# Kernel tuning notes

Measured on AMD Instinct MI355X. Metric: run time of the kernel, lower is better.

## Reference

```python
import jax, jax.numpy as jnp
import numpy as np
from jax import lax

NUM_CLASSES = 2
TOP_K = 200
CONF_THRESH = 0.01
NMS_THRESH = 0.45
VAR0, VAR1 = 0.1, 0.2  # SSD cfg['variance']
BATCH, NUM_PRIORS = 8, 4096


def setup_inputs() -> dict:
    key = jax.random.key(0)
    k1, k2, k3, k4 = jax.random.split(key, 4)
    loc_data = jax.random.normal(k1, (BATCH, NUM_PRIORS, 4), dtype=jnp.float32)
    conf_data = jax.random.normal(k2, (BATCH * NUM_PRIORS, NUM_CLASSES), dtype=jnp.float32)
    # priors: (cx, cy, w, h), centers in [0,1], sizes in [0.02, 0.3]
    centers = jax.random.uniform(k3, (NUM_PRIORS, 2), dtype=jnp.float32)
    sizes = jax.random.uniform(k4, (NUM_PRIORS, 2), dtype=jnp.float32, minval=0.02, maxval=0.3)
    prior_data = jnp.concatenate([centers, sizes], axis=1)
    return {"loc_data": loc_data, "conf_data": conf_data, "prior_data": prior_data}


def _pairwise_iou(boxes):
    # boxes: [N, 4] in (x1, y1, x2, y2)
    x1, y1, x2, y2 = boxes[:, 0], boxes[:, 1], boxes[:, 2], boxes[:, 3]
    area = (x2 - x1) * (y2 - y1)
    iw = jnp.maximum(jnp.minimum(x2[:, None], x2[None, :]) - jnp.maximum(x1[:, None], x1[None, :]), 0.0)
    ih = jnp.maximum(jnp.minimum(y2[:, None], y2[None, :]) - jnp.maximum(y1[:, None], y1[None, :]), 0.0)
    inter = iw * ih
    return inter / (area[:, None] + area[None, :] - inter)


def _nms_image(boxes, scores):
    # boxes [N,4], scores [N] -> [TOP_K, 5] rows of (score, x1, y1, x2, y2)
    N = scores.shape[0]
    order = jnp.argsort(-scores)
    b = boxes[order]
    s = scores[order]
    valid = s > CONF_THRESH  # conf threshold (c_mask in torch code)
    iou = _pairwise_iou(b)  # [N, N]

    def step(suppressed, xs):
        i, row, v = xs
        kept_i = v & jnp.logical_not(suppressed[i])
        suppressed = suppressed | (kept_i & (row > NMS_THRESH))
        return suppressed, kept_i

    _, kept = lax.scan(step, jnp.zeros((N,), bool), (jnp.arange(N), iou, valid))
    # scatter kept rows (in descending-score order) into the first <=TOP_K slots
    pos = jnp.cumsum(kept.astype(jnp.int32)) - 1
    rows = jnp.concatenate([s[:, None], b], axis=1)  # [N, 5]
    idx = jnp.where(kept & (pos < TOP_K), pos, TOP_K)  # invalid rows -> dump slot
    out = jnp.zeros((TOP_K + 1, 5), dtype=boxes.dtype).at[idx].set(rows)
    return out[:TOP_K]


def reference(loc_data, conf_data, prior_data):
    B = loc_data.shape[0]
    N = prior_data.shape[0]
    conf = jax.nn.softmax(conf_data, axis=-1).reshape(B, N, NUM_CLASSES)
    scores = conf[:, :, 1]  # objectness (class 1)
    # SSD decode (vectorized over batch)
    cxcy = prior_data[None, :, :2] + loc_data[..., :2] * VAR0 * prior_data[None, :, 2:]
    wh = prior_data[None, :, 2:] * jnp.exp(loc_data[..., 2:] * VAR1)
    boxes = jnp.concatenate([cxcy - wh * 0.5, cxcy + wh * 0.5], axis=-1)  # [B, N, 4]
    per_img = jax.vmap(_nms_image)(boxes, scores)  # [B, TOP_K, 5]
    out = jnp.zeros((B, NUM_CLASSES, TOP_K, 5), dtype=loc_data.dtype)
    out = out.at[:, 1].set(per_img)  # class 0 (background) stays zero
    return out
```

## Files before the change

kernel.cpp:

```cpp
#include <hip/hip_runtime.h>
#include <math.h>

#define BATCH 8
#define NPRI  4096
#define TOPK  200

typedef unsigned long long u64;
typedef unsigned int u32;

#define WS_SOA (BATCH * NPRI)

__device__ __forceinline__ float exp_f32_cr(float x) { return (float)exp((double)x); }

__global__ __launch_bounds__(256) void rank_decode_kernel(
    const float* __restrict__ loc, const float* __restrict__ conf,
    const float* __restrict__ prior, float* __restrict__ ws) {
  __shared__ u64 sk[NPRI];
  __shared__ u32 prank[8][128];
  const int blk = blockIdx.x;
  const int b = blk >> 5;
  const int tile = blk & 31;
  const int t = threadIdx.x;
  const int ig = t & 31;
  const int rg = t >> 5;

  {
    const float2* cf = (const float2*)conf + b * NPRI;
#pragma unroll 4
    for (int g = t; g < NPRI; g += 256) {
      float2 c = cf[g];
      float m  = fmaxf(c.x, c.y);
      float e0 = exp_f32_cr(__fsub_rn(c.x, m));
      float e1 = exp_f32_cr(__fsub_rn(c.y, m));
      float s  = __fdiv_rn(e1, __fadd_rn(e0, e1));
      sk[g] = ((u64)(~__float_as_uint(s)) << 32) | (u32)g;
    }
  }
  __syncthreads();

  const ulonglong2* sk2 = (const ulonglong2*)sk;
  const ulonglong2 pA = sk2[tile * 64 + ig * 2];
  const ulonglong2 pB = sk2[tile * 64 + ig * 2 + 1];
  const u64 k0 = pA.x, k1 = pA.y, k2 = pB.x, k3 = pB.y;
  u32 c0 = 0, c1 = 0, c2 = 0, c3 = 0;
  {
    const int r0 = rg * 256;
#pragma unroll 4
    for (int r = r0; r < r0 + 256; ++r) {
      ulonglong2 kk = sk2[r];
      c0 += (kk.x < k0); c0 += (kk.y < k0);
      c1 += (kk.x < k1); c1 += (kk.y < k1);
      c2 += (kk.x < k2); c2 += (kk.y < k2);
      c3 += (kk.x < k3); c3 += (kk.y < k3);
    }
  }
  ((uint4*)prank[rg])[ig] = make_uint4(c0, c1, c2, c3);
  __syncthreads();

  if (t < 128) {
    int rank = 0;
#pragma unroll
    for (int q = 0; q < 8; ++q) rank += (int)prank[q][t];
    const int ig2 = tile * 128 + t;
    const u64 myk = sk[ig2];
    const float s = __uint_as_float(~(u32)(myk >> 32));
    const float4 l = ((const float4*)loc)[b * NPRI + ig2];
    const float4 pq = ((const float4*)prior)[ig2];
    float cx = __fadd_rn(pq.x, __fmul_rn(__fmul_rn(l.x, 0.1f), pq.z));
    float cy = __fadd_rn(pq.y, __fmul_rn(__fmul_rn(l.y, 0.1f), pq.w));
    float w  = __fmul_rn(pq.z, exp_f32_cr(__fmul_rn(l.z, 0.2f)));
    float h  = __fmul_rn(pq.w, exp_f32_cr(__fmul_rn(l.w, 0.2f)));
    float hw = __fmul_rn(w, 0.5f), hh = __fmul_rn(h, 0.5f);
    float x1 = __fsub_rn(cx, hw), x2 = __fadd_rn(cx, hw);
    float y1 = __fsub_rn(cy, hh), y2 = __fadd_rn(cy, hh);
    const int o = b * NPRI + rank;
    float* sx1 = ws;
    float* sy1 = ws + 1 * WS_SOA;
    float* sx2 = ws + 2 * WS_SOA;
    float* sy2 = ws + 3 * WS_SOA;
    float* sar = ws + 4 * WS_SOA;
    float* ssc = ws + 5 * WS_SOA;
    sx1[o] = x1; sy1[o] = y1; sx2[o] = x2; sy2[o] = y2;
    sar[o] = __fmul_rn(__fsub_rn(x2, x1), __fsub_rn(y2, y1));
    ssc[o] = s;
  }
}

__global__ __launch_bounds__(512) void nms_scan_kernel(const float* __restrict__ ws,
                                                       float* __restrict__ out) {
  __shared__ float4 kbox[TOPK];
  __shared__ float  karea[TOPK];
  __shared__ float4 bx[64];
  __shared__ float  ba[64];
  __shared__ u64 diag[64];
  __shared__ u64 parts[8];
  __shared__ int klist[TOPK];
  __shared__ int s_kcnt, s_cnt, s_stop, s_total;

  const int b = blockIdx.x, t = threadIdx.x, lane = t & 63, wv = t >> 6;
  const float* sx1 = ws;
  const float* sy1 = ws + 1 * WS_SOA;
  const float* sx2 = ws + 2 * WS_SOA;
  const float* sy2 = ws + 3 * WS_SOA;
  const float* sar = ws + 4 * WS_SOA;
  const float* ssc = ws + 5 * WS_SOA;
  const double M = 0.5 * ((double)0.45f + (double)__uint_as_float(0x3EE66667u));

  float* slice = out + (size_t)b * 2 * TOPK * 5;
  for (int p = t; p < 2 * TOPK * 5; p += 512) slice[p] = 0.0f;

  if (t == 0) { s_kcnt = 0; s_cnt = 0; s_stop = 0; s_total = 0; }

  int o_n = b * NPRI + lane;
  float nx1 = sx1[o_n], ny1 = sy1[o_n], nx2 = sx2[o_n], ny2 = sy2[o_n];
  float nar = sar[o_n], nsc = ssc[o_n];
  __syncthreads();

  for (int c = 0; c < 64; ++c) {
    const int col = c * 64 + lane, o = b * NPRI + col;
    const float x1 = nx1, y1 = ny1, x2 = nx2, y2 = ny2, ar = nar, sc = nsc;
    if (c + 1 < 64) {
      const int on = o + 64;
      nx1 = sx1[on]; ny1 = sy1[on]; nx2 = sx2[on]; ny2 = sy2[on];
      nar = sar[on]; nsc = ssc[on];
    }
    const int kcnt = s_kcnt;
    if (wv == 0) { bx[lane] = make_float4(x1, y1, x2, y2); ba[lane] = ar; }
    __syncthreads();

    bool supp = false;
    for (int k = wv; k < kcnt; k += 8) {
      float4 kb = kbox[k]; float ka = karea[k];
      float iw = fmaxf(__fsub_rn(fminf(kb.z, x2), fmaxf(kb.x, x1)), 0.0f);
      float ih = fmaxf(__fsub_rn(fminf(kb.w, y2), fmaxf(kb.y, y1)), 0.0f);
      float inter = __fmul_rn(iw, ih);
      float uni   = __fsub_rn(__fadd_rn(ka, ar), inter);
      if ((double)inter > M * (double)uni) { supp = true; break; }
    }
    u64 bw = __ballot(supp);
    if (lane == 0) parts[wv] = bw;

#pragma unroll
    for (int r = 8 * wv; r < 8 * wv + 8; ++r) {
      float4 rb = bx[r]; float ra = ba[r];
      float iw = fmaxf(__fsub_rn(fminf(rb.z, x2), fmaxf(rb.x, x1)), 0.0f);
      float ih = fmaxf(__fsub_rn(fminf(rb.w, y2), fmaxf(rb.y, y1)), 0.0f);
      float inter = __fmul_rn(iw, ih);
      float uni   = __fsub_rn(__fadd_rn(ra, ar), inter);
      u64 dw = __ballot((double)inter > M * (double)uni);
      if (lane == 0) diag[r] = dw;
    }
    __syncthreads();

    if (wv == 0) {
      u64 vm = __ballot(sc > 0.01f);
      int cnt = s_cnt;
      bool stop = false;
      if (vm == 0) {
        stop = true;
      } else {
        u64 rw = parts[0] | parts[1] | parts[2] | parts[3] |
                 parts[4] | parts[5] | parts[6] | parts[7];
        u64 ck = 0;
        for (int g = 0; g < 64; g += 8) {
          u64 d[8];
#pragma unroll
          for (int q = 0; q < 8; ++q) d[q] = diag[g + q];
#pragma unroll
          for (int q = 0; q < 8; ++q) {
            u64 kbit = ((vm & ~rw) >> (g + q)) & 1ull;
            rw |= d[q] & (0ull - kbit);
            ck |= kbit << (g + q);
          }
        }
        if ((ck >> lane) & 1ull) {
          int pos = cnt + __popcll(ck & ((1ull << lane) - 1ull));
          if (pos < TOPK) {
            klist[pos] = col;
            kbox[pos] = make_float4(x1, y1, x2, y2);
            karea[pos] = ar;
          }
        }
        cnt += __popcll(ck);
        if (cnt >= TOPK) stop = true;
      }
      if (lane == 0) {
        int capped = cnt < TOPK ? cnt : TOPK;
        s_kcnt = capped; s_cnt = cnt; s_total = capped; s_stop = stop ? 1 : 0;
      }
    }
    __syncthreads();
    if (s_stop) break;
  }

  const int total = s_total;
  for (int p = t; p < total; p += 512) {
    int i = klist[p];
    int o = b * NPRI + i;
    float* dst = out + (((size_t)b * 2 + 1) * TOPK + p) * 5;
    dst[0] = ssc[o]; dst[1] = sx1[o]; dst[2] = sy1[o]; dst[3] = sx2[o]; dst[4] = sy2[o];
  }
}

extern "C" void kernel_launch(void* const* d_in, const int* in_sizes, int n_in,
                              void* d_out, int out_size, void* d_ws, size_t ws_size,
                              hipStream_t stream) {
  const float* loc   = (const float*)d_in[0];
  const float* conf  = (const float*)d_in[1];
  const float* prior = (const float*)d_in[2];
  float* out = (float*)d_out;
  float* ws  = (float*)d_ws;

  rank_decode_kernel<<<256, 256, 0, stream>>>(loc, conf, prior, ws);
  nms_scan_kernel<<<BATCH, 512, 0, stream>>>(ws, out);
}
```

Measured before the change: 90.01 us.

## Remove per-chunk barrier in NMS scan and rebalance rank counting

```diff
diff --git a/kernel.cpp b/kernel.cpp
--- a/kernel.cpp
+++ b/kernel.cpp
@@ -14,15 +14,21 @@
 
 __global__ __launch_bounds__(256) void rank_decode_kernel(
     const float* __restrict__ loc, const float* __restrict__ conf,
-    const float* __restrict__ prior, float* __restrict__ ws) {
+    const float* __restrict__ prior, float* __restrict__ ws,
+    float* __restrict__ out) {
   __shared__ u64 sk[NPRI];
-  __shared__ u32 prank[8][128];
+  __shared__ u32 prank[16][128];
   const int blk = blockIdx.x;
   const int b = blk >> 5;
   const int tile = blk & 31;
   const int t = threadIdx.x;
-  const int ig = t & 31;
-  const int rg = t >> 5;
+  const int rg = t >> 4;
+  const int ig = t & 15;
+
+  if (tile == 0) {
+    float* slice = out + (size_t)b * 2 * TOPK * 5;
+    for (int p = t; p < 2 * TOPK * 5; p += 256) slice[p] = 0.0f;
+  }
 
   {
     const float2* cf = (const float2*)conf + b * NPRI;
@@ -30,37 +36,43 @@
     for (int g = t; g < NPRI; g += 256) {
       float2 c = cf[g];
       float m  = fmaxf(c.x, c.y);
-      float e0 = exp_f32_cr(__fsub_rn(c.x, m));
-      float e1 = exp_f32_cr(__fsub_rn(c.y, m));
-      float s  = __fdiv_rn(e1, __fadd_rn(e0, e1));
+      float a  = __fadd_rn(__fsub_rn(c.x, m), __fsub_rn(c.y, m));
+      float e  = exp_f32_cr(a);
+      float s  = (c.y >= c.x) ? __fdiv_rn(1.0f, __fadd_rn(e, 1.0f))
+                              : __fdiv_rn(e, __fadd_rn(1.0f, e));
       sk[g] = ((u64)(~__float_as_uint(s)) << 32) | (u32)g;
     }
   }
   __syncthreads();
 
   const ulonglong2* sk2 = (const ulonglong2*)sk;
-  const ulonglong2 pA = sk2[tile * 64 + ig * 2];
-  const ulonglong2 pB = sk2[tile * 64 + ig * 2 + 1];
-  const u64 k0 = pA.x, k1 = pA.y, k2 = pB.x, k3 = pB.y;
-  u32 c0 = 0, c1 = 0, c2 = 0, c3 = 0;
+  u64 K[8];
+#pragma unroll
+  for (int q = 0; q < 4; ++q) {
+    ulonglong2 p = sk2[tile * 64 + ig * 4 + q];
+    K[2 * q] = p.x; K[2 * q + 1] = p.y;
+  }
+  u32 C[8] = {0, 0, 0, 0, 0, 0, 0, 0};
   {
-    const int r0 = rg * 256;
-#pragma unroll 4
-    for (int r = r0; r < r0 + 256; ++r) {
+    const int r0 = rg * 128;
+#pragma unroll 2
+    for (int r = r0; r < r0 + 128; ++r) {
       ulonglong2 kk = sk2[r];
-      c0 += (kk.x < k0); c0 += (kk.y < k0);
-      c1 += (kk.x < k1); c1 += (kk.y < k1);
-      c2 += (kk.x < k2); c2 += (kk.y < k2);
-      c3 += (kk.x < k3); c3 += (kk.y < k3);
-    }
-  }
-  ((uint4*)prank[rg])[ig] = make_uint4(c0, c1, c2, c3);
+#pragma unroll
+      for (int q = 0; q < 8; ++q) {
+        C[q] += (kk.x < K[q]);
+        C[q] += (kk.y < K[q]);
+      }
+    }
+  }
+  ((uint4*)prank[rg])[ig * 2 + 0] = make_uint4(C[0], C[1], C[2], C[3]);
+  ((uint4*)prank[rg])[ig * 2 + 1] = make_uint4(C[4], C[5], C[6], C[7]);
   __syncthreads();
 
   if (t < 128) {
     int rank = 0;
 #pragma unroll
-    for (int q = 0; q < 8; ++q) rank += (int)prank[q][t];
+    for (int q = 0; q < 16; ++q) rank += (int)prank[q][t];
     const int ig2 = tile * 128 + t;
     const u64 myk = sk[ig2];
     const float s = __uint_as_float(~(u32)(myk >> 32));
@@ -106,14 +118,12 @@
   const float* ssc = ws + 5 * WS_SOA;
   const double M = 0.5 * ((double)0.45f + (double)__uint_as_float(0x3EE66667u));
 
-  float* slice = out + (size_t)b * 2 * TOPK * 5;
-  for (int p = t; p < 2 * TOPK * 5; p += 512) slice[p] = 0.0f;
-
   if (t == 0) { s_kcnt = 0; s_cnt = 0; s_stop = 0; s_total = 0; }
 
   int o_n = b * NPRI + lane;
   float nx1 = sx1[o_n], ny1 = sy1[o_n], nx2 = sx2[o_n], ny2 = sy2[o_n];
   float nar = sar[o_n], nsc = ssc[o_n];
+  if (wv == 0) { bx[lane] = make_float4(nx1, ny1, nx2, ny2); ba[lane] = nar; }
   __syncthreads();
 
   for (int c = 0; c < 64; ++c) {
@@ -125,8 +135,6 @@
       nar = sar[on]; nsc = ssc[on];
     }
     const int kcnt = s_kcnt;
-    if (wv == 0) { bx[lane] = make_float4(x1, y1, x2, y2); ba[lane] = ar; }
-    __syncthreads();
 
     bool supp = false;
     for (int k = wv; k < kcnt; k += 8) {
@@ -152,6 +160,10 @@
     }
     __syncthreads();
 
+    if (wv == 1 && c + 1 < 64) {
+      bx[lane] = make_float4(nx1, ny1, nx2, ny2);
+      ba[lane] = nar;
+    }
     if (wv == 0) {
       u64 vm = __ballot(sc > 0.01f);
       int cnt = s_cnt;
@@ -211,6 +223,6 @@
   float* out = (float*)d_out;
   float* ws  = (float*)d_ws;
 
-  rank_decode_kernel<<<256, 256, 0, stream>>>(loc, conf, prior, ws);
+  rank_decode_kernel<<<256, 256, 0, stream>>>(loc, conf, prior, ws, out);
   nms_scan_kernel<<<BATCH, 512, 0, stream>>>(ws, out);
 }
```

After: 90.08 us. About the same (+0.1%).
